# Performance work log

Measured on AMD Instinct MI355X. Metric: run time of the kernel, lower is better.

The kernel has to match this reference:

```python
import jax, jax.numpy as jnp
import numpy as np

T, C, H, W = 16, 3, 480, 864
N_PIX = 2_000_000


def setup_inputs() -> dict:
    key = jax.random.key(0)
    k1, k2 = jax.random.split(key)
    samples = jax.random.normal(k1, (T, C, H, W), dtype=jnp.float32)
    encoded_pixels = jax.random.randint(k2, (1, T, H, W), 0, N_PIX, dtype=jnp.int32)
    return {"samples": samples, "encoded_pixels": encoded_pixels, "n_pixels": N_PIX}


def reference(samples, encoded_pixels, n_pixels):
    # samples: [T, 3, H0, W0] float32; encoded_pixels: [1, T, Hc, Wc] int32
    Hc, Wc = encoded_pixels.shape[-2:]
    H0, W0 = samples.shape[-2:]
    Tn, Cn = samples.shape[0], samples.shape[1]

    # F.interpolate(mode='bilinear', align_corners=False) == jax.image.resize bilinear w/o antialias
    s = jax.image.resize(samples, (Tn, Cn, Hc, Wc), method='bilinear', antialias=False)
    s = jnp.transpose(s, (0, 2, 3, 1)).astype(jnp.float16)  # [T, Hc, Wc, 3]

    idx = encoded_pixels[0].reshape(-1)  # [T*Hc*Wc]

    # scatter-add values and counts into the unique-pixel buffer (segment sum)
    vals = jax.ops.segment_sum(s.reshape(-1, Cn), idx, num_segments=n_pixels)       # [n_pixels, 3] fp16
    counts = jax.ops.segment_sum(jnp.ones_like(idx), idx, num_segments=n_pixels)    # [n_pixels] int32
    counts = counts[:, None]

    # segment mean where count > 0, else raw accumulated (zero) value
    pixels = jnp.where(counts > 0, vals / counts.astype(vals.dtype), vals)

    # gather back per-frame and resize to the original shape
    mixed = pixels[idx].reshape(Tn, Hc, Wc, Cn)          # [T, Hc, Wc, 3]
    mixed = jnp.transpose(mixed, (0, 3, 1, 2))           # [T, 3, Hc, Wc]
    mixed = jax.image.resize(mixed, (Tn, Cn, H0, W0), method='bilinear', antialias=False)
    return mixed
```

## Files before the change

kernel.cpp:

```cpp
#include <hip/hip_runtime.h>
#include <hip/hip_fp16.h>

#define T_   16
#define C_   3
#define H_   480
#define W_   864
#define HW_  (H_ * W_)
#define CHW_ (C_ * HW_)
#define NPOS (T_ * HW_)
#define NPIX 2000000


#define FBITS 19
#define FMASK ((1ULL << FBITS) - 1)
#define BIAS  2048
#define QSCALE 256.0f

#define BBITS  12
#define NBIN   (1 << BBITS)
#define NBUCK  489
#define SLOTS  15360

#define PTHREADS 512
#define PITEMS   10

#define SK 8
#define GK 8
#define GV 4

#define GITEMS 16
#define NSLICE 8
#define SLICE_SHIFT 18

typedef unsigned long long u64;
typedef unsigned int       u32;
typedef int   int4v   __attribute__((ext_vector_type(4)));
typedef float float4v __attribute__((ext_vector_type(4)));

__device__ __forceinline__ unsigned int q8b(float v) {
    float h = __half2float(__float2half(v));
    h = fminf(fmaxf(h, -7.9f), 7.9f);
    return (unsigned int)(__float2int_rn(h * QSCALE) + BIAS);
}

__device__ __forceinline__ u64 decode_pack(u64 s) {
    u32 k = (u32)(s >> 57);
    float a = 0.f, bb = 0.f, cc = 0.f;
    if (k) {
        float bias = (float)(int)(k * BIAS);
        float inv  = 1.0f / (QSCALE * (float)k);
        a  = ((float)(int)( s                 & FMASK) - bias) * inv;
        bb = ((float)(int)((s >>  FBITS)      & FMASK) - bias) * inv;
        cc = ((float)(int)((s >> (2 * FBITS)) & FMASK) - bias) * inv;
    }
    return  (u64)__half_as_ushort(__float2half(a))
         | ((u64)__half_as_ushort(__float2half(bb)) << 16)
         | ((u64)__half_as_ushort(__float2half(cc)) << 32);
}


__global__ __launch_bounds__(256) void zero_table(ulonglong2* __restrict__ t, int n2)
{
    int i = blockIdx.x * 256 + threadIdx.x;
    int stride = gridDim.x * 256;
    for (; i < n2; i += stride) t[i] = make_ulonglong2(0ULL, 0ULL);
}

__global__ __launch_bounds__(512) void zero_counters(u32* __restrict__ c)
{
    int i = threadIdx.x;
    if (i < NBUCK) c[i] = 0;
}


__global__ __launch_bounds__(PTHREADS) void partition_kernel(
    const float* __restrict__ samples,
    const int*   __restrict__ enc,
    u64* __restrict__ region,
    u32* __restrict__ counters)
{
    __shared__ u64 stage[PTHREADS * PITEMS];
    __shared__ u32 lh[PTHREADS], le[PTHREADS], gp[PTHREADS];
    __shared__ u32 wsum[8];

    const int t    = threadIdx.x;
    const int lane = t & 63;
    const int wid  = t >> 6;
    const int base = blockIdx.x * (PTHREADS * PITEMS);

    lh[t] = 0;
    __syncthreads();

    u64 rec[PITEMS];
    u32 bkt[PITEMS], rnk[PITEMS];
    #pragma unroll
    for (int k = 0; k < PITEMS; ++k) {
        int j  = base + k * PTHREADS + t;
        int p  = __builtin_nontemporal_load(&enc[j]);
        int tt = j / HW_;
        int hw = j - tt * HW_;
        const float* sp = samples + (size_t)tt * CHW_ + hw;
        u32 c0 = q8b(__builtin_nontemporal_load(&sp[0]));
        u32 c1 = q8b(__builtin_nontemporal_load(&sp[HW_]));
        u32 c2 = q8b(__builtin_nontemporal_load(&sp[2 * HW_]));
        rec[k] = (u64)(u32)p | ((u64)c0 << 21) | ((u64)c1 << 33) | ((u64)c2 << 45);
        bkt[k] = (u32)p >> BBITS;
        rnk[k] = atomicAdd(&lh[bkt[k]], 1u);
    }
    __syncthreads();

    u32 x = lh[t];
    #pragma unroll
    for (int d = 1; d < 64; d <<= 1) {
        u32 y = __shfl_up(x, d, 64);
        if (lane >= d) x += y;
    }
    if (lane == 63) wsum[wid] = x;
    __syncthreads();
    u32 off = 0;
    #pragma unroll
    for (int w = 0; w < 8; ++w)
        off += (w < wid) ? wsum[w] : 0u;
    le[t] = x + off - lh[t];
    if (t < NBUCK) gp[t] = atomicAdd(&counters[t], lh[t]);
    __syncthreads();

    #pragma unroll
    for (int k = 0; k < PITEMS; ++k)
        stage[le[bkt[k]] + rnk[k]] = rec[k];
    __syncthreads();

    #pragma unroll
    for (int k = 0; k < PITEMS; ++k) {
        int idx = k * PTHREADS + t;
        u64 rc  = stage[idx];
        u32 b   = ((u32)rc & 0x1FFFFFu) >> BBITS;
        u32 pos = gp[b] + ((u32)idx - le[b]);
        if (pos < SLOTS)
            __builtin_nontemporal_store(rc, &region[(size_t)b * SLOTS + pos]);
    }
}

__global__ __launch_bounds__(1024) void accum_kernel(
    const u64* __restrict__ region,
    const u32* __restrict__ counters,
    u64* __restrict__ tpk)
{
    __shared__ u64 bins[NBIN];
    const int b = blockIdx.x, t = threadIdx.x;

    for (int i = t; i < NBIN; i += 1024) bins[i] = 0ULL;
    __syncthreads();

    u32 n = counters[b]; if (n > SLOTS) n = SLOTS;
    const u64* rp = region + (size_t)b * SLOTS;
    for (u32 i = t; i < n; i += 1024) {
        u64 rc = __builtin_nontemporal_load(&rp[i]);
        u64 d  =  ((rc >> 21) & 0xFFFULL)
               | (((rc >> 33) & 0xFFFULL) << FBITS)
               | (((rc >> 45) & 0xFFFULL) << (2 * FBITS))
               | (1ULL << 57);
        atomicAdd(&bins[(u32)rc & (NBIN - 1)], d);
    }
    __syncthreads();

    for (int i = t; i < NBIN; i += 1024) {
        int pix = (b << BBITS) + i;
        if (pix >= NPIX) break;
        tpk[pix] = decode_pack(bins[i]);
    }
}


__global__ __launch_bounds__(256) void gather_phased(
    const int* __restrict__ enc,
    const u64* __restrict__ tpk,
    float* __restrict__ out)
{
    const int tid  = threadIdx.x;
    const int base = blockIdx.x * (GITEMS * 256);

    u32 e[GITEMS];
    #pragma unroll
    for (int it = 0; it < GITEMS; ++it)
        e[it] = (u32)__builtin_nontemporal_load(&enc[base + it * 256 + tid]);

    u64 v[GITEMS];
    for (int s = 0; s < NSLICE; ++s) {
        #pragma unroll
        for (int it = 0; it < GITEMS; ++it) {
            if ((e[it] >> SLICE_SHIFT) == (u32)s)
                v[it] = tpk[e[it]];
        }
    }

    #pragma unroll
    for (int it = 0; it < GITEMS; ++it) {
        int j  = base + it * 256 + tid;
        int t  = j / HW_;
        int hw = j - t * HW_;
        float* ob = out + (size_t)t * CHW_ + hw;
        __builtin_nontemporal_store(
            __half2float(__ushort_as_half((unsigned short)(v[it]      ))), &ob[0]);
        __builtin_nontemporal_store(
            __half2float(__ushort_as_half((unsigned short)(v[it] >> 16))), &ob[HW_]);
        __builtin_nontemporal_store(
            __half2float(__ushort_as_half((unsigned short)(v[it] >> 32))), &ob[2 * HW_]);
    }
}


__global__ __launch_bounds__(256) void gather_all(
    const int* __restrict__ enc,
    const u64* __restrict__ tpk,
    float* __restrict__ out)
{
    const int q0 = blockIdx.x * (GV * 256) + threadIdx.x;
    const int4v* enc4 = (const int4v*)enc;

    int4v e[GV];
    #pragma unroll
    for (int k = 0; k < GV; ++k)
        e[k] = __builtin_nontemporal_load(&enc4[q0 + k * 256]);

    u64 v[GV][4];
    #pragma unroll
    for (int k = 0; k < GV; ++k) {
        v[k][0] = tpk[e[k][0]];
        v[k][1] = tpk[e[k][1]];
        v[k][2] = tpk[e[k][2]];
        v[k][3] = tpk[e[k][3]];
    }

    #pragma unroll
    for (int k = 0; k < GV; ++k) {
        int q  = q0 + k * 256;
        int j  = q * 4;
        int t  = j / HW_;
        int hw = j - t * HW_;
        float* ob = out + (size_t)t * CHW_ + hw;
        #pragma unroll
        for (int c = 0; c < 3; ++c) {
            float4v o;
            o[0] = __half2float(__ushort_as_half((unsigned short)(v[k][0] >> (16 * c))));
            o[1] = __half2float(__ushort_as_half((unsigned short)(v[k][1] >> (16 * c))));
            o[2] = __half2float(__ushort_as_half((unsigned short)(v[k][2] >> (16 * c))));
            o[3] = __half2float(__ushort_as_half((unsigned short)(v[k][3] >> (16 * c))));
            __builtin_nontemporal_store(o, (float4v*)(ob + (size_t)c * HW_));
        }
    }
}


__global__ __launch_bounds__(256) void scatter_kernel(
    const float* __restrict__ samples,
    const int*   __restrict__ enc,
    u64* __restrict__ table)
{
    const int j0 = blockIdx.x * (SK * 256) + threadIdx.x;
    int   p [SK];
    float s0[SK], s1[SK], s2[SK];
    #pragma unroll
    for (int k = 0; k < SK; ++k) p[k] = enc[j0 + k * 256];
    #pragma unroll
    for (int k = 0; k < SK; ++k) {
        int j  = j0 + k * 256;
        int t  = j / HW_;
        int hw = j - t * HW_;
        const float* sp = samples + (size_t)t * CHW_ + hw;
        s0[k] = sp[0]; s1[k] = sp[HW_]; s2[k] = sp[2 * HW_];
    }
    #pragma unroll
    for (int k = 0; k < SK; ++k) {
        u64 d = (u64)q8b(s0[k]) | ((u64)q8b(s1[k]) << FBITS)
              | ((u64)q8b(s2[k]) << (2 * FBITS)) | (1ULL << 57);
        atomicAdd(table + p[k], d);
    }
}

__global__ __launch_bounds__(256) void merge_kernel(
    const u64* __restrict__ table,
    u64* __restrict__ tpk)
{
    int i = blockIdx.x * 256 + threadIdx.x;
    if (i >= NPIX) return;
    tpk[i] = decode_pack(table[i]);
}

__global__ __launch_bounds__(256) void gather_legacy(
    const int* __restrict__ enc,
    const u64* __restrict__ table,
    float* __restrict__ out)
{
    const int j20 = blockIdx.x * (GK * 256) + threadIdx.x;
    int2 pp[GK];
    #pragma unroll
    for (int k = 0; k < GK; ++k)
        pp[k] = reinterpret_cast<const int2*>(enc)[j20 + k * 256];
    u64 sa[GK], sb[GK];
    #pragma unroll
    for (int k = 0; k < GK; ++k) { sa[k] = table[pp[k].x]; sb[k] = table[pp[k].y]; }
    float2* out2 = reinterpret_cast<float2*>(out);
    #pragma unroll
    for (int k = 0; k < GK; ++k) {
        const int j = (j20 + k * 256) * 2;
        u32 ka = (u32)(sa[k] >> 57), kb = (u32)(sb[k] >> 57);
        float biasa = (float)(int)(ka * BIAS), biasb = (float)(int)(kb * BIAS);
        float inva = 1.0f / (QSCALE * (float)ka), invb = 1.0f / (QSCALE * (float)kb);
        int t  = j / HW_;
        int hw = j - t * HW_;
        size_t obase = (size_t)t * CHW_ + hw;
        float2 o;
        o.x = __half2float(__float2half(((float)(int)( sa[k]                 & FMASK) - biasa) * inva));
        o.y = __half2float(__float2half(((float)(int)( sb[k]                 & FMASK) - biasb) * invb));
        out2[(obase) >> 1] = o;
        o.x = __half2float(__float2half(((float)(int)((sa[k] >> FBITS)       & FMASK) - biasa) * inva));
        o.y = __half2float(__float2half(((float)(int)((sb[k] >> FBITS)       & FMASK) - biasb) * invb));
        out2[(obase + HW_) >> 1] = o;
        o.x = __half2float(__float2half(((float)(int)((sa[k] >> (2 * FBITS)) & FMASK) - biasa) * inva));
        o.y = __half2float(__float2half(((float)(int)((sb[k] >> (2 * FBITS)) & FMASK) - biasb) * invb));
        out2[(obase + 2 * HW_) >> 1] = o;
    }
}


extern "C" void kernel_launch(void* const* d_in, const int* in_sizes, int n_in,
                              void* d_out, int out_size, void* d_ws, size_t ws_size,
                              hipStream_t stream) {
    const float* samples = nullptr;
    const int*   enc     = nullptr;
    for (int i = 0; i < n_in; ++i) {
        if (in_sizes[i] == T_ * C_ * HW_)      samples = (const float*)d_in[i];
        else if (in_sizes[i] == T_ * HW_)      enc     = (const int*)d_in[i];
    }
    float* out = (float*)d_out;

    const size_t regionB = (size_t)NBUCK * SLOTS * 8;
    const size_t ctrOff  = regionB;
    const size_t tabOff  = regionB + 2048;
    const size_t fullNeed = tabOff + (size_t)NPIX * 8;

    const size_t tblB    = (size_t)NPIX * 8;
    const size_t midNeed = tblB + (size_t)NPIX * 8;

    if (ws_size >= fullNeed) {
        u64* region = (u64*)d_ws;
        u32* ctr    = (u32*)((char*)d_ws + ctrOff);
        u64* tpk    = (u64*)((char*)d_ws + tabOff);

        zero_counters<<<dim3(1), dim3(512), 0, stream>>>(ctr);
        partition_kernel<<<dim3(NPOS / (PTHREADS * PITEMS)), dim3(PTHREADS), 0, stream>>>(
            samples, enc, region, ctr);
        accum_kernel<<<dim3(NBUCK), dim3(1024), 0, stream>>>(region, ctr, tpk);
        gather_phased<<<dim3(NPOS / (GITEMS * 256)), dim3(256), 0, stream>>>(enc, tpk, out);
    } else if (ws_size >= midNeed) {
        u64* table = (u64*)d_ws;
        u64* tpk   = (u64*)((char*)d_ws + tblB);

        zero_table<<<dim3(2048), dim3(256), 0, stream>>>((ulonglong2*)table, NPIX / 2);
        scatter_kernel<<<dim3(NPOS / (SK * 256)), dim3(256), 0, stream>>>(samples, enc, table);
        merge_kernel<<<dim3((NPIX + 255) / 256), dim3(256), 0, stream>>>(table, tpk);
        gather_all<<<dim3(NPOS / 4 / (GV * 256)), dim3(256), 0, stream>>>(enc, tpk, out);
    } else {
        u64* table = (u64*)d_ws;
        zero_table<<<dim3(2048), dim3(256), 0, stream>>>((ulonglong2*)table, NPIX / 2);
        scatter_kernel<<<dim3(NPOS / (SK * 256)), dim3(256), 0, stream>>>(samples, enc, table);
        gather_legacy<<<dim3(NPOS / 2 / (GK * 256)), dim3(256), 0, stream>>>(enc, table, out);
    }
}
```

Baseline: 305.0 us.

## Fuse accumulation and gather into one kernel with a software grid barrier

Merges the per-bucket accumulation kernel and the phased gather kernel into one launch. A global atomic counter, reset by zero_counters, acts as a grid-wide barrier between decoding the packed table and gathering it back to the output. After the barrier the 489 blocks of 1024 threads each gather 14 strided items in two tiles. This removes one kernel launch and the tail gap between kernels, but it needs all 489 blocks resident at once (launch bounds ask for 8 blocks per unit) or the barrier deadlocks. The gather also runs with fewer threads than the separate kernel used.

```diff
diff --git a/kernel.cpp b/kernel.cpp
--- a/kernel.cpp
+++ b/kernel.cpp
@@ -28,9 +28,11 @@
 #define GK 8
 #define GV 4
 
-#define GITEMS 16
 #define NSLICE 8
 #define SLICE_SHIFT 18
+
+#define NTH   (NBUCK * 1024)
+#define GTILE 7
 
 typedef unsigned long long u64;
 typedef unsigned int       u32;
@@ -69,7 +71,7 @@
 __global__ __launch_bounds__(512) void zero_counters(u32* __restrict__ c)
 {
     int i = threadIdx.x;
-    if (i < NBUCK) c[i] = 0;
+    if (i <= NBUCK) c[i] = 0;
 }
 
 
@@ -141,10 +143,13 @@
     }
 }
 
-__global__ __launch_bounds__(1024) void accum_kernel(
+
+__global__ __launch_bounds__(1024, 8) void accum_gather(
     const u64* __restrict__ region,
-    const u32* __restrict__ counters,
-    u64* __restrict__ tpk)
+    u32* __restrict__ counters,
+    u64* __restrict__ tpk,
+    const int* __restrict__ enc,
+    float* __restrict__ out)
 {
     __shared__ u64 bins[NBIN];
     const int b = blockIdx.x, t = threadIdx.x;
@@ -166,49 +171,91 @@
 
     for (int i = t; i < NBIN; i += 1024) {
         int pix = (b << BBITS) + i;
-        if (pix >= NPIX) break;
-        tpk[pix] = decode_pack(bins[i]);
-    }
-}
-
-
-__global__ __launch_bounds__(256) void gather_phased(
-    const int* __restrict__ enc,
-    const u64* __restrict__ tpk,
-    float* __restrict__ out)
-{
-    const int tid  = threadIdx.x;
-    const int base = blockIdx.x * (GITEMS * 256);
-
-    u32 e[GITEMS];
-    #pragma unroll
-    for (int it = 0; it < GITEMS; ++it)
-        e[it] = (u32)__builtin_nontemporal_load(&enc[base + it * 256 + tid]);
-
-    u64 v[GITEMS];
-    for (int s = 0; s < NSLICE; ++s) {
+        if (pix < NPIX) tpk[pix] = decode_pack(bins[i]);
+    }
+
+    __threadfence();
+    __syncthreads();
+    u32* bar = counters + NBUCK;
+    if (t == 0) {
+        __hip_atomic_fetch_add(bar, 1u, __ATOMIC_ACQ_REL, __HIP_MEMORY_SCOPE_AGENT);
+        while (__hip_atomic_load(bar, __ATOMIC_ACQUIRE, __HIP_MEMORY_SCOPE_AGENT) < NBUCK)
+            __builtin_amdgcn_s_sleep(8);
+    }
+    __syncthreads();
+    __threadfence();
+
+    const int gtid = b * 1024 + t;
+
+    #pragma unroll
+    for (int tile = 0; tile < 2; ++tile) {
+        u32 e[GTILE];
+        u64 v[GTILE];
         #pragma unroll
-        for (int it = 0; it < GITEMS; ++it) {
-            if ((e[it] >> SLICE_SHIFT) == (u32)s)
-                v[it] = tpk[e[it]];
+        for (int it = 0; it < GTILE; ++it) {
+            int j = (tile * GTILE + it) * NTH + gtid;
+            e[it] = (j < NPOS) ? (u32)__builtin_nontemporal_load(&enc[j])
+                               : 0xFFFFFFFFu;
         }
-    }
-
-    #pragma unroll
-    for (int it = 0; it < GITEMS; ++it) {
-        int j  = base + it * 256 + tid;
+        for (int s = 0; s < NSLICE; ++s) {
+            #pragma unroll
+            for (int it = 0; it < GTILE; ++it)
+                if ((e[it] >> SLICE_SHIFT) == (u32)s)
+                    v[it] = tpk[e[it]];
+        }
+        #pragma unroll
+        for (int it = 0; it < GTILE; ++it) {
+            int j = (tile * GTILE + it) * NTH + gtid;
+            if (j < NPOS) {
+                int tt = j / HW_;
+                int hw = j - tt * HW_;
+                float* ob = out + (size_t)tt * CHW_ + hw;
+                __builtin_nontemporal_store(
+                    __half2float(__ushort_as_half((unsigned short)(v[it]      ))), &ob[0]);
+                __builtin_nontemporal_store(
+                    __half2float(__ushort_as_half((unsigned short)(v[it] >> 16))), &ob[HW_]);
+                __builtin_nontemporal_store(
+                    __half2float(__ushort_as_half((unsigned short)(v[it] >> 32))), &ob[2 * HW_]);
+            }
+        }
+    }
+}
+
+
+__global__ __launch_bounds__(256) void scatter_kernel(
+    const float* __restrict__ samples,
+    const int*   __restrict__ enc,
+    u64* __restrict__ table)
+{
+    const int j0 = blockIdx.x * (SK * 256) + threadIdx.x;
+    int   p [SK];
+    float s0[SK], s1[SK], s2[SK];
+    #pragma unroll
+    for (int k = 0; k < SK; ++k) p[k] = enc[j0 + k * 256];
+    #pragma unroll
+    for (int k = 0; k < SK; ++k) {
+        int j  = j0 + k * 256;
         int t  = j / HW_;
         int hw = j - t * HW_;
-        float* ob = out + (size_t)t * CHW_ + hw;
-        __builtin_nontemporal_store(
-            __half2float(__ushort_as_half((unsigned short)(v[it]      ))), &ob[0]);
-        __builtin_nontemporal_store(
-            __half2float(__ushort_as_half((unsigned short)(v[it] >> 16))), &ob[HW_]);
-        __builtin_nontemporal_store(
-            __half2float(__ushort_as_half((unsigned short)(v[it] >> 32))), &ob[2 * HW_]);
-    }
-}
-
+        const float* sp = samples + (size_t)t * CHW_ + hw;
+        s0[k] = sp[0]; s1[k] = sp[HW_]; s2[k] = sp[2 * HW_];
+    }
+    #pragma unroll
+    for (int k = 0; k < SK; ++k) {
+        u64 d = (u64)q8b(s0[k]) | ((u64)q8b(s1[k]) << FBITS)
+              | ((u64)q8b(s2[k]) << (2 * FBITS)) | (1ULL << 57);
+        atomicAdd(table + p[k], d);
+    }
+}
+
+__global__ __launch_bounds__(256) void merge_kernel(
+    const u64* __restrict__ table,
+    u64* __restrict__ tpk)
+{
+    int i = blockIdx.x * 256 + threadIdx.x;
+    if (i >= NPIX) return;
+    tpk[i] = decode_pack(table[i]);
+}
 
 __global__ __launch_bounds__(256) void gather_all(
     const int* __restrict__ enc,
@@ -249,42 +296,6 @@
             __builtin_nontemporal_store(o, (float4v*)(ob + (size_t)c * HW_));
         }
     }
-}
-
-
-__global__ __launch_bounds__(256) void scatter_kernel(
-    const float* __restrict__ samples,
-    const int*   __restrict__ enc,
-    u64* __restrict__ table)
-{
-    const int j0 = blockIdx.x * (SK * 256) + threadIdx.x;
-    int   p [SK];
-    float s0[SK], s1[SK], s2[SK];
-    #pragma unroll
-    for (int k = 0; k < SK; ++k) p[k] = enc[j0 + k * 256];
-    #pragma unroll
-    for (int k = 0; k < SK; ++k) {
-        int j  = j0 + k * 256;
-        int t  = j / HW_;
-        int hw = j - t * HW_;
-        const float* sp = samples + (size_t)t * CHW_ + hw;
-        s0[k] = sp[0]; s1[k] = sp[HW_]; s2[k] = sp[2 * HW_];
-    }
-    #pragma unroll
-    for (int k = 0; k < SK; ++k) {
-        u64 d = (u64)q8b(s0[k]) | ((u64)q8b(s1[k]) << FBITS)
-              | ((u64)q8b(s2[k]) << (2 * FBITS)) | (1ULL << 57);
-        atomicAdd(table + p[k], d);
-    }
-}
-
-__global__ __launch_bounds__(256) void merge_kernel(
-    const u64* __restrict__ table,
-    u64* __restrict__ tpk)
-{
-    int i = blockIdx.x * 256 + threadIdx.x;
-    if (i >= NPIX) return;
-    tpk[i] = decode_pack(table[i]);
 }
 
 __global__ __launch_bounds__(256) void gather_legacy(
@@ -351,8 +362,8 @@
         zero_counters<<<dim3(1), dim3(512), 0, stream>>>(ctr);
         partition_kernel<<<dim3(NPOS / (PTHREADS * PITEMS)), dim3(PTHREADS), 0, stream>>>(
             samples, enc, region, ctr);
-        accum_kernel<<<dim3(NBUCK), dim3(1024), 0, stream>>>(region, ctr, tpk);
-        gather_phased<<<dim3(NPOS / (GITEMS * 256)), dim3(256), 0, stream>>>(enc, tpk, out);
+        accum_gather<<<dim3(NBUCK), dim3(1024), 0, stream>>>(
+            region, ctr, tpk, enc, out);
     } else if (ws_size >= midNeed) {
         u64* table = (u64*)d_ws;
         u64* tpk   = (u64*)((char*)d_ws + tblB);
```

Result: slower. 633.7 us (+107.8%).
